# Kernel tuning notes

Hardware: AMD Instinct MI355X
Metric: run time of the kernel (lower is better)

## Reference

```python
import jax, jax.numpy as jnp
import numpy as np

H = 512
NHALF = 32  # N // 2 complex conjugate pairs
LLEN = 8192


def setup_inputs() -> dict:
    key = jax.random.key(0)
    k1, k2, k3 = jax.random.split(key, 3)
    # log_dt ~ uniform in [log(dt_min), log(dt_max)]
    log_dt = jax.random.uniform(k1, (H,), dtype=jnp.float32) * (
        np.log(0.1) - np.log(0.001)) + np.log(0.001)
    # C: complex randn stored as (H, NHALF, 2) real view
    C = jax.random.normal(k2, (H, NHALF, 2), dtype=jnp.float32)
    log_A_real = jnp.log(0.5 * jnp.ones((H, NHALF), dtype=jnp.float32))
    A_imag = np.pi * jnp.broadcast_to(
        jnp.arange(NHALF, dtype=jnp.float32), (H, NHALF))
    return {"C": C, "log_dt": log_dt, "log_A_real": log_A_real,
            "A_imag": A_imag, "L": LLEN}


def reference(C, log_dt, log_A_real, A_imag, L):
    # zoh discretization of diagonal SSM -> kernel K of shape (H, L)
    dt = jnp.exp(log_dt)                                  # (H,)
    Cc = (C[..., 0] + 1j * C[..., 1]).astype(jnp.complex64)  # (H, n)
    A = (-jnp.exp(log_A_real) + 1j * A_imag).astype(jnp.complex64)  # (H, n)
    dtA = A * dt[:, None]                                 # (H, n)
    t = jnp.arange(L, dtype=jnp.float32)                  # (L,)
    C_scaled = Cc * (jnp.exp(dtA) - 1.0) / A              # (H, n)
    # Vandermonde: exp(dtA)^t over length L, reduce over n
    T = jnp.exp(dtA[:, :, None] * t[None, None, :])       # (H, n, L) complex
    K = 2.0 * jnp.einsum('hn,hnl->hl', C_scaled, T).real  # (H, L)
    return K
```

## Files before the change

kernel.cpp:

```cpp
#include <hip/hip_runtime.h>
#include <math.h>

#define HDIM   512
#define NH     32
#define LLEN   8192
#define BLOCK  256
#define LSPLIT 2
#define LPB    (LLEN / LSPLIT)
#define LPT    16

__global__ __launch_bounds__(BLOCK) void s4d_kernel(
    const float* __restrict__ C,
    const float* __restrict__ log_dt,
    const float* __restrict__ log_A_real,
    const float* __restrict__ A_imag,
    float* __restrict__ out)
{
    __shared__ float2 tabA[NH][16];
    __shared__ float2 tabB[NH][16];
    __shared__ float4 s_cw[NH];
    __shared__ float2 s_pq[NH];

    const int h   = blockIdx.y;
    const int ls  = blockIdx.x;
    const int tid = threadIdx.x;

    {
        const int n = tid & 31;
        const int g = tid >> 5;
        const double dt  = exp((double)log_dt[h]);
        const double Are = -exp((double)log_A_real[h * NH + n]);
        const double Aim = (double)A_imag[h * NH + n];
        const double dre = Are * dt, dim = Aim * dt;

        const bool   isB  = (g >= 4);
        const int    i0   = (isB ? (g - 4) : g) * 4;
        const double step = isB ? 256.0 : 16.0;
        const double base = isB ? ((double)(LPB * ls) + 256.0 * (double)i0)
                                : (16.0 * (double)i0);

        double s0, c0; sincos(dim * base, &s0, &c0);
        const double m0 = exp(dre * base);
        double er = m0 * c0, ei = m0 * s0;
        double ss, cs; sincos(dim * step, &ss, &cs);
        const double ms = exp(dre * step);
        const double str = ms * cs, sti = ms * ss;

        float2* dst = isB ? &tabB[n][0] : &tabA[n][0];
        for (int k = 0; k < 4; ++k) {
            dst[i0 + k] = make_float2((float)er, (float)ei);
            const double t = er * str - ei * sti;
            ei = er * sti + ei * str;
            er = t;
        }

        if (g == 0) {
            double s1, c1; sincos(dim, &s1, &c1);
            const double em  = exp(dre);
            const double w1r = em * c1, w1i = em * s1;
            const double nre = w1r - 1.0, nim = w1i;
            const double den = Are * Are + Aim * Aim;
            const double fre = (nre * Are + nim * Aim) / den;
            const double fim = (nim * Are - nre * Aim) / den;
            const double Cre = (double)C[(h * NH + n) * 2 + 0];
            const double Cim = (double)C[(h * NH + n) * 2 + 1];
            s_cw[n] = make_float4((float)(2.0 * (Cre * fre - Cim * fim)),
                                  (float)(2.0 * (Cre * fim + Cim * fre)),
                                  (float)w1r, (float)w1i);
            s_pq[n] = make_float2((float)(2.0 * w1r), (float)(em * em));
        }
    }
    __syncthreads();

    const int lo = tid & 15, hi = tid >> 4;

    float acc[LPT];
#pragma unroll
    for (int l = 0; l < LPT; ++l) acc[l] = 0.0f;

#pragma unroll 1
    for (int n = 0; n < NH; n += 2) {
        const float2 Aa = tabA[n][lo],     Ba = tabB[n][hi];
        const float2 Ab = tabA[n + 1][lo], Bb = tabB[n + 1][hi];
        const float4 cwa = s_cw[n], cwb = s_cw[n + 1];
        const float2 pqa = s_pq[n], pqb = s_pq[n + 1];

        const float Tar = fmaf(Aa.x, Ba.x, -(Aa.y * Ba.y));
        const float Tai = fmaf(Aa.x, Ba.y,   Aa.y * Ba.x);
        const float Tbr = fmaf(Ab.x, Bb.x, -(Ab.y * Bb.y));
        const float Tbi = fmaf(Ab.x, Bb.y,   Ab.y * Bb.x);

        float ypa = fmaf(cwa.x, Tar, -(cwa.y * Tai));
        float ypb = fmaf(cwb.x, Tbr, -(cwb.y * Tbi));

        const float T1ar = fmaf(Tar, cwa.z, -(Tai * cwa.w));
        const float T1ai = fmaf(Tar, cwa.w,   Tai * cwa.z);
        const float T1br = fmaf(Tbr, cwb.z, -(Tbi * cwb.w));
        const float T1bi = fmaf(Tbr, cwb.w,   Tbi * cwb.z);

        float ya = fmaf(cwa.x, T1ar, -(cwa.y * T1ai));
        float yb = fmaf(cwb.x, T1br, -(cwb.y * T1bi));

        acc[0] += ypa + ypb;
        acc[1] += ya  + yb;

#pragma unroll
        for (int l = 2; l < LPT; ++l) {
            const float za = fmaf(pqa.x, ya, -(pqa.y * ypa));
            const float zb = fmaf(pqb.x, yb, -(pqb.y * ypb));
            acc[l] += za + zb;
            ypa = ya; ya = za;
            ypb = yb; yb = zb;
        }
    }

    float* orow = out + (size_t)h * LLEN + ls * LPB + LPT * tid;
#pragma unroll
    for (int j = 0; j < 4; ++j) {
        *(float4*)(orow + 4 * j) =
            make_float4(acc[4*j], acc[4*j+1], acc[4*j+2], acc[4*j+3]);
    }
}

extern "C" void kernel_launch(void* const* d_in, const int* in_sizes, int n_in,
                              void* d_out, int out_size, void* d_ws, size_t ws_size,
                              hipStream_t stream) {
    const float* C          = (const float*)d_in[0];
    const float* log_dt     = (const float*)d_in[1];
    const float* log_A_real = (const float*)d_in[2];
    const float* A_imag     = (const float*)d_in[3];
    float* out = (float*)d_out;

    dim3 grid(LSPLIT, HDIM);
    s4d_kernel<<<grid, BLOCK, 0, stream>>>(C, log_dt, log_A_real, A_imag, out);
}
```

Measured before the change: 80.98 us.

## Pack mode pairs into float2 vectors, fold C scale into table, use stride-2 recurrence

```diff
diff --git a/kernel.cpp b/kernel.cpp
--- a/kernel.cpp
+++ b/kernel.cpp
@@ -3,11 +3,15 @@
 
 #define HDIM   512
 #define NH     32
+#define NP     16
 #define LLEN   8192
 #define BLOCK  256
 #define LSPLIT 2
 #define LPB    (LLEN / LSPLIT)
 #define LPT    16
+
+typedef float vf2 __attribute__((ext_vector_type(2)));
+#define VFMA(a, b, c) __builtin_elementwise_fma((a), (b), (c))
 
 __global__ __launch_bounds__(BLOCK) void s4d_kernel(
     const float* __restrict__ C,
@@ -16,10 +20,11 @@
     const float* __restrict__ A_imag,
     float* __restrict__ out)
 {
-    __shared__ float2 tabA[NH][16];
-    __shared__ float2 tabB[NH][16];
-    __shared__ float4 s_cw[NH];
-    __shared__ float2 s_pq[NH];
+    __shared__ float4 tabA[NP][16];
+    __shared__ float4 tabB[NP][16];
+    __shared__ float4 s_w [NP];
+    __shared__ float4 s_pq[NP];
+    __shared__ float4 s_p2[NP];
 
     const int h   = blockIdx.y;
     const int ls  = blockIdx.x;
@@ -28,97 +33,132 @@
     {
         const int n = tid & 31;
         const int g = tid >> 5;
+        const int P = n >> 1, o = n & 1;
         const double dt  = exp((double)log_dt[h]);
         const double Are = -exp((double)log_A_real[h * NH + n]);
         const double Aim = (double)A_imag[h * NH + n];
         const double dre = Are * dt, dim = Aim * dt;
 
-        const bool   isB  = (g >= 4);
-        const int    i0   = (isB ? (g - 4) : g) * 4;
-        const double step = isB ? 256.0 : 16.0;
-        const double base = isB ? ((double)(LPB * ls) + 256.0 * (double)i0)
-                                : (16.0 * (double)i0);
+        double s1, c1; sincos(dim, &s1, &c1);
+        const double em  = exp(dre);
+        const double w1r = em * c1, w1i = em * s1;
 
-        double s0, c0; sincos(dim * base, &s0, &c0);
-        const double m0 = exp(dre * base);
-        double er = m0 * c0, ei = m0 * s0;
-        double ss, cs; sincos(dim * step, &ss, &cs);
-        const double ms = exp(dre * step);
-        const double str = ms * cs, sti = ms * ss;
+        float* tabAf = (float*)&tabA[0][0];
+        float* tabBf = (float*)&tabB[0][0];
 
-        float2* dst = isB ? &tabB[n][0] : &tabA[n][0];
-        for (int k = 0; k < 4; ++k) {
-            dst[i0 + k] = make_float2((float)er, (float)ei);
-            const double t = er * str - ei * sti;
-            ei = er * sti + ei * str;
-            er = t;
-        }
-
-        if (g == 0) {
-            double s1, c1; sincos(dim, &s1, &c1);
-            const double em  = exp(dre);
-            const double w1r = em * c1, w1i = em * s1;
+        if (g < 4) {
             const double nre = w1r - 1.0, nim = w1i;
             const double den = Are * Are + Aim * Aim;
             const double fre = (nre * Are + nim * Aim) / den;
             const double fim = (nim * Are - nre * Aim) / den;
             const double Cre = (double)C[(h * NH + n) * 2 + 0];
             const double Cim = (double)C[(h * NH + n) * 2 + 1];
-            s_cw[n] = make_float4((float)(2.0 * (Cre * fre - Cim * fim)),
-                                  (float)(2.0 * (Cre * fim + Cim * fre)),
-                                  (float)w1r, (float)w1i);
-            s_pq[n] = make_float2((float)(2.0 * w1r), (float)(em * em));
+            const double csr = 2.0 * (Cre * fre - Cim * fim);
+            const double csi = 2.0 * (Cre * fim + Cim * fre);
+
+            const int    i0   = g * 4;
+            const double base = 16.0 * (double)i0;
+            double s0, c0; sincos(dim * base, &s0, &c0);
+            const double m0 = exp(dre * base);
+            const double er = m0 * c0, ei = m0 * s0;
+            double gr = csr * er - csi * ei;
+            double gi = csr * ei + csi * er;
+            double ss, cs; sincos(dim * 16.0, &ss, &cs);
+            const double ms  = exp(dre * 16.0);
+            const double str = ms * cs, sti = ms * ss;
+            for (int k = 0; k < 4; ++k) {
+                const int idx = (P * 16 + i0 + k) * 4;
+                tabAf[idx + o]     = (float)gr;
+                tabAf[idx + 2 + o] = (float)gi;
+                const double t = gr * str - gi * sti;
+                gi = gr * sti + gi * str;
+                gr = t;
+            }
+        } else {
+            const int    i0   = (g - 4) * 4;
+            const double base = (double)(LPB * ls) + 256.0 * (double)i0;
+            double s0, c0; sincos(dim * base, &s0, &c0);
+            const double m0 = exp(dre * base);
+            double er = m0 * c0, ei = m0 * s0;
+            double ss, cs; sincos(dim * 256.0, &ss, &cs);
+            const double ms  = exp(dre * 256.0);
+            const double str = ms * cs, sti = ms * ss;
+            for (int k = 0; k < 4; ++k) {
+                const int idx = (P * 16 + i0 + k) * 4;
+                tabBf[idx + o]     = (float)er;
+                tabBf[idx + 2 + o] = (float)ei;
+                const double t = er * str - ei * sti;
+                ei = er * sti + ei * str;
+                er = t;
+            }
+        }
+
+        if (g == 0) {
+            float* wf  = (float*)&s_w[0];
+            float* pqf = (float*)&s_pq[0];
+            float* p2f = (float*)&s_p2[0];
+            const double p  = 2.0 * w1r;
+            const double q  = em * em;
+            const double p2 = 2.0 * (w1r * w1r - w1i * w1i);
+            const double q2 = q * q;
+            wf [P * 4 + o]     = (float)w1r;
+            wf [P * 4 + 2 + o] = (float)w1i;
+            pqf[P * 4 + o]     = (float)p;
+            pqf[P * 4 + 2 + o] = (float)q;
+            p2f[P * 4 + o]     = (float)p2;
+            p2f[P * 4 + 2 + o] = (float)q2;
         }
     }
     __syncthreads();
 
     const int lo = tid & 15, hi = tid >> 4;
 
-    float acc[LPT];
+    vf2 acc[LPT];
 #pragma unroll
-    for (int l = 0; l < LPT; ++l) acc[l] = 0.0f;
+    for (int l = 0; l < LPT; ++l) acc[l] = (vf2)(0.f);
 
-#pragma unroll 1
-    for (int n = 0; n < NH; n += 2) {
-        const float2 Aa = tabA[n][lo],     Ba = tabB[n][hi];
-        const float2 Ab = tabA[n + 1][lo], Bb = tabB[n + 1][hi];
-        const float4 cwa = s_cw[n], cwb = s_cw[n + 1];
-        const float2 pqa = s_pq[n], pqb = s_pq[n + 1];
+#pragma unroll 2
+    for (int P = 0; P < NP; ++P) {
+        const float4 a4  = tabA[P][lo];
+        const float4 b4  = tabB[P][hi];
+        const float4 w4  = s_w[P];
+        const float4 pq4 = s_pq[P];
+        const float4 p24 = s_p2[P];
 
-        const float Tar = fmaf(Aa.x, Ba.x, -(Aa.y * Ba.y));
-        const float Tai = fmaf(Aa.x, Ba.y,   Aa.y * Ba.x);
-        const float Tbr = fmaf(Ab.x, Bb.x, -(Ab.y * Bb.y));
-        const float Tbi = fmaf(Ab.x, Bb.y,   Ab.y * Bb.x);
+        const vf2 Ax = {a4.x, a4.y}, Ay = {a4.z, a4.w};
+        const vf2 Bx = {b4.x, b4.y}, By = {b4.z, b4.w};
+        const vf2 wr = {w4.x, w4.y}, wi = {w4.z, w4.w};
+        const vf2 p  = {pq4.x, pq4.y}, q  = {pq4.z, pq4.w};
+        const vf2 p2 = {p24.x, p24.y}, q2 = {p24.z, p24.w};
 
-        float ypa = fmaf(cwa.x, Tar, -(cwa.y * Tai));
-        float ypb = fmaf(cwb.x, Tbr, -(cwb.y * Tbi));
+        const vf2 Tr = VFMA(Ax, Bx, -(Ay * By));
+        const vf2 Ti = VFMA(Ax, By,  (Ay * Bx));
+        const vf2 y0 = Tr;
+        const vf2 y1 = VFMA(Tr, wr, -(Ti * wi));
+        const vf2 y2 = VFMA(p, y1, -(q * y0));
+        const vf2 y3 = VFMA(p, y2, -(q * y1));
+        acc[0] += y0; acc[1] += y1; acc[2] += y2; acc[3] += y3;
 
-        const float T1ar = fmaf(Tar, cwa.z, -(Tai * cwa.w));
-        const float T1ai = fmaf(Tar, cwa.w,   Tai * cwa.z);
-        const float T1br = fmaf(Tbr, cwb.z, -(Tbi * cwb.w));
-        const float T1bi = fmaf(Tbr, cwb.w,   Tbi * cwb.z);
-
-        float ya = fmaf(cwa.x, T1ar, -(cwa.y * T1ai));
-        float yb = fmaf(cwb.x, T1br, -(cwb.y * T1bi));
-
-        acc[0] += ypa + ypb;
-        acc[1] += ya  + yb;
-
+        vf2 e0 = y0, e1 = y2, o0 = y1, o1 = y3;
 #pragma unroll
-        for (int l = 2; l < LPT; ++l) {
-            const float za = fmaf(pqa.x, ya, -(pqa.y * ypa));
-            const float zb = fmaf(pqb.x, yb, -(pqb.y * ypb));
-            acc[l] += za + zb;
-            ypa = ya; ya = za;
-            ypb = yb; yb = zb;
+        for (int m = 0; m < 6; ++m) {
+            const vf2 e2 = VFMA(p2, e1, -(q2 * e0));
+            const vf2 o2 = VFMA(p2, o1, -(q2 * o0));
+            acc[4 + 2 * m] += e2;
+            acc[5 + 2 * m] += o2;
+            e0 = e1; e1 = e2;
+            o0 = o1; o1 = o2;
         }
     }
 
     float* orow = out + (size_t)h * LLEN + ls * LPB + LPT * tid;
 #pragma unroll
     for (int j = 0; j < 4; ++j) {
-        *(float4*)(orow + 4 * j) =
-            make_float4(acc[4*j], acc[4*j+1], acc[4*j+2], acc[4*j+3]);
+        *(float4*)(orow + 4 * j) = make_float4(
+            acc[4*j+0].x + acc[4*j+0].y,
+            acc[4*j+1].x + acc[4*j+1].y,
+            acc[4*j+2].x + acc[4*j+2].y,
+            acc[4*j+3].x + acc[4*j+3].y);
     }
 }
 
```

After: 81.12 us. About the same (+0.2%).
